# Performance work log

Measured on AMD Instinct MI355X. Metric: run time of the kernel, lower is better.

## Reference

```python
import jax, jax.numpy as jnp
import numpy as np

B, N, C = 8, 4096, 512
H = W = 64           # N = H * W, dimensionality == 2
SHIFT = 4            # shift_size
WS = 8               # window_size
R = 4                # mlp_ratio
EPS = 1e-6


def setup_inputs() -> dict:
    key = jax.random.key(0)
    ks = jax.random.split(key, 3)
    return {
        "inputs": jax.random.normal(ks[0], (B, N, C), dtype=jnp.float32),
        # second_norm (LayerNormalization) params
        "ln_gamma": jnp.ones((C,), jnp.float32),
        "ln_beta": jnp.zeros((C,), jnp.float32),
        # MLP params: Dense(C*R) -> gelu -> Dense(C)
        "W1": jax.random.normal(ks[1], (C, C * R), dtype=jnp.float32) * 0.02,
        "b1": jnp.zeros((C * R,), jnp.float32),
        "W2": jax.random.normal(ks[2], (C * R, C), dtype=jnp.float32) * 0.02,
        "b2": jnp.zeros((C,), jnp.float32),
    }


def _layer_norm(x, gamma, beta):
    mu = jnp.mean(x, axis=-1, keepdims=True)
    var = jnp.mean(jnp.square(x - mu), axis=-1, keepdims=True)
    return (x - mu) * jax.lax.rsqrt(var + EPS) * gamma + beta


def reference(inputs, ln_gamma, ln_beta, W1, b1, W2, b2):
    # NOTE: faithful to the provided call(): first_norm and attention are
    # never invoked (`normed = x`, `self_att = windowed`), so the window
    # partition + reverse is an exact identity round-trip of the shifted grid.
    grid = inputs.reshape(B, H, W, C)
    shifted = jnp.roll(grid, (-SHIFT, -SHIFT), axis=(1, 2))  # SwinCyclicShifter

    # window partition: [B, nH, nW, WS, WS, C] windows of WSxWS patches
    nh = H // WS
    win = shifted.reshape(B, nh, WS, nh, WS, C).transpose(0, 1, 3, 2, 4, 5)
    # (identity "attention" on [B*nH*nW, WS*WS, C]) then window reverse
    unwin = win.transpose(0, 1, 3, 2, 4, 5).reshape(B, N, C)

    x = unwin + inputs                       # residual add
    normed = _layer_norm(x, ln_gamma, ln_beta)
    h = jax.nn.gelu(normed @ W1 + b1)        # [B, N, 4C]
    mlp_out = h @ W2 + b2                    # [B, N, C]
    return mlp_out + x
```

## Files before the change

### kernel.cpp

```cpp
#include <hip/hip_runtime.h>
#include <hip/hip_bf16.h>
#include <cstdint>
#include <cstddef>


typedef short bf16x8 __attribute__((ext_vector_type(8)));
typedef float f32x4 __attribute__((ext_vector_type(4)));

#define GLOBAL_AS(p) ((__attribute__((address_space(1))) void*)(uintptr_t)(p))
#define LDS_AS(p)    ((__attribute__((address_space(3))) void*)(p))

static __device__ __forceinline__ ushort f2bf(float f) {
    uint32_t u = __float_as_uint(f);
    uint32_t r = (u + 0x7FFFu + ((u >> 16) & 1u)) >> 16;
    return (ushort)r;
}

static __device__ __forceinline__ float gelu_e2(float v) {
    float v2 = v * v;
    float m = fmaf(-0.1029433f, v2, -2.3022084f);
    float t = v * m;
    float e;
    asm("v_exp_f32 %0, %1" : "=v"(e) : "v"(t));
    return v * __builtin_amdgcn_rcpf(1.0f + e);
}

static __device__ __forceinline__ int rolled_row(int row) {
    int b = row >> 12, n = row & 4095;
    int h = n >> 6, wv = n & 63;
    int n2 = (((h + 4) & 63) << 6) | ((wv + 4) & 63);
    return (b << 12) | n2;
}

#define SBAR() do { __builtin_amdgcn_sched_barrier(0); \
                    __builtin_amdgcn_s_barrier(); \
                    __builtin_amdgcn_sched_barrier(0); } while (0)

#define LBAR() do { __builtin_amdgcn_sched_barrier(0); \
                    asm volatile("s_waitcnt lgkmcnt(0)" ::: "memory"); \
                    __builtin_amdgcn_s_barrier(); \
                    __builtin_amdgcn_sched_barrier(0); } while (0)

__global__ __launch_bounds__(128)
void ln_kernel(const float* __restrict__ in, const float* __restrict__ gamma,
               const float* __restrict__ beta, ushort* __restrict__ normed) {
    const int row = blockIdx.x;
    const int t = threadIdx.x;
    const int row2 = rolled_row(row);

    const float4* p0 = (const float4*)(in + (size_t)row * 512);
    const float4* p1 = (const float4*)(in + (size_t)row2 * 512);
    float4 a = p0[t], c = p1[t];
    float x0 = a.x + c.x, x1 = a.y + c.y, x2 = a.z + c.z, x3 = a.w + c.w;

    float s = x0 + x1 + x2 + x3;
    float sq = x0 * x0 + x1 * x1 + x2 * x2 + x3 * x3;
#pragma unroll
    for (int o = 32; o > 0; o >>= 1) {
        s += __shfl_xor(s, o);
        sq += __shfl_xor(sq, o);
    }
    __shared__ float red[4];
    if ((t & 63) == 0) { red[(t >> 6) * 2] = s; red[(t >> 6) * 2 + 1] = sq; }
    __syncthreads();
    s = red[0] + red[2];
    sq = red[1] + red[3];
    float mu = s * (1.0f / 512.0f);
    float var = sq * (1.0f / 512.0f) - mu * mu;
    float rs = rsqrtf(var + 1e-6f);

    float4 g = ((const float4*)gamma)[t];
    float4 be = ((const float4*)beta)[t];
    ushort4 o4;
    o4.x = f2bf((x0 - mu) * rs * g.x + be.x);
    o4.y = f2bf((x1 - mu) * rs * g.y + be.y);
    o4.z = f2bf((x2 - mu) * rs * g.z + be.z);
    o4.w = f2bf((x3 - mu) * rs * g.w + be.w);
    ((ushort4*)(normed + (size_t)row * 512))[t] = o4;
}

template <int PERM>
__global__ __launch_bounds__(256)
void transpose_cast(const float* __restrict__ src, ushort* __restrict__ dst,
                    int R, int Ccols) {
    __shared__ float tile[32][33];
    const int bx = blockIdx.x * 32;
    const int by = blockIdx.y * 32;
    const int tx = threadIdx.x, ty = threadIdx.y;
#pragma unroll
    for (int i = 0; i < 32; i += 8)
        tile[ty + i][tx] = src[(size_t)(by + ty + i) * Ccols + bx + tx];
    __syncthreads();
    int k = by + tx;
    int kd = PERM ? ((k & ~63) | ((k & 15) << 2) | ((k >> 4) & 3)) : k;
#pragma unroll
    for (int i = 0; i < 32; i += 8)
        dst[(size_t)(bx + ty + i) * R + kd] = f2bf(tile[tx][ty + i]);
}

__global__ __launch_bounds__(256)
void mlp_gemm1(const ushort* __restrict__ A, const ushort* __restrict__ Bt,
               const float* __restrict__ bias, ushort* __restrict__ outH) {
    constexpr int K = 512, N = 2048, BK = 64;
    __shared__ ushort Asm[128 * BK];
    __shared__ ushort Bsm[128 * BK];

    const int t = threadIdx.x;
    const int w = t >> 6, l = t & 63;
    const int wr = w >> 1, wc = w & 1;

    const int bid = blockIdx.x;
    const int xcd = bid & 7, idx = bid >> 3;
    const int brow = ((xcd << 5) + (idx >> 4)) << 7;
    const int bcol = (idx & 15) << 7;

    f32x4 acc[4][4] = {};

    const int trow = t >> 3;
    const int csrc = (((t & 7) ^ ((t >> 3) & 7)) << 3);
    const size_t aBase = (size_t)(brow + trow) * K + csrc;
    const size_t bBase = (size_t)(bcol + trow) * K + csrc;
    char* const ldsA = (char*)Asm + w * 1024;
    char* const ldsB = (char*)Bsm + w * 1024;

    const int rA = l & 15;
    const int cb0 = ((l >> 4) ^ (rA & 7)) << 4;
    const int bA0 = (wr << 13) + (rA << 7) + cb0;
    const int bB0 = (wc << 13) + (rA << 7) + cb0;
    const char* const pA0 = (const char*)Asm + bA0;
    const char* const pA1 = (const char*)Asm + (bA0 ^ 64);
    const char* const pB0 = (const char*)Bsm + bB0;
    const char* const pB1 = (const char*)Bsm + (bB0 ^ 64);

    for (int k0 = 0; k0 < K; k0 += BK) {
#pragma unroll
        for (int i = 0; i < 4; ++i) {
            __builtin_amdgcn_global_load_lds(GLOBAL_AS(A + aBase + (size_t)(i * 32) * K + k0),
                                             LDS_AS(ldsA + i * 4096), 16, 0, 0);
            __builtin_amdgcn_global_load_lds(GLOBAL_AS(Bt + bBase + (size_t)(i * 32) * K + k0),
                                             LDS_AS(ldsB + i * 4096), 16, 0, 0);
        }
        __syncthreads();

#pragma unroll
        for (int s = 0; s < 2; ++s) {
            const char* pa = s ? pA1 : pA0;
            const char* pb = s ? pB1 : pB0;
            bf16x8 aF[4], bF[4];
#pragma unroll
            for (int i = 0; i < 4; ++i)
                aF[i] = *(const bf16x8*)(pa + i * 2048);
#pragma unroll
            for (int j = 0; j < 4; ++j)
                bF[j] = *(const bf16x8*)(pb + j * 2048);
#pragma unroll
            for (int i = 0; i < 4; ++i)
#pragma unroll
                for (int j = 0; j < 4; ++j)
                    acc[i][j] = __builtin_amdgcn_mfma_f32_16x16x32_bf16(aF[i], bF[j], acc[i][j], 0, 0, 0);
        }
        __syncthreads();
    }

    const int cm = (l >> 4) << 2;
    const int cn = l & 15;
    float bvv[4];
#pragma unroll
    for (int j = 0; j < 4; ++j)
        bvv[j] = bias[bcol + wc * 64 + j * 16 + cn];
    const int ecol = bcol + wc * 64 + (cn << 2);
#pragma unroll
    for (int i = 0; i < 4; ++i) {
#pragma unroll
        for (int r = 0; r < 4; ++r) {
            const int row = brow + wr * 64 + i * 16 + cm + r;
            float f0 = gelu_e2(acc[i][0][r] + bvv[0]);
            float f1 = gelu_e2(acc[i][1][r] + bvv[1]);
            float f2 = gelu_e2(acc[i][2][r] + bvv[2]);
            float f3 = gelu_e2(acc[i][3][r] + bvv[3]);
            uint32_t lo, hi;
            asm("v_cvt_pk_bf16_f32 %0, %1, %2" : "=v"(lo) : "v"(f0), "v"(f1));
            asm("v_cvt_pk_bf16_f32 %0, %1, %2" : "=v"(hi) : "v"(f2), "v"(f3));
            uint2 pv; pv.x = lo; pv.y = hi;
            *(uint2*)(outH + (size_t)row * N + ecol) = pv;
        }
    }
}

__global__ __launch_bounds__(512, 2)
void mlp_gemm2(const ushort* __restrict__ A, const ushort* __restrict__ Bt,
               const float* __restrict__ bias, const float* __restrict__ resid,
               float* __restrict__ outF) {
    constexpr int KT = 2048, TT = 32, N = 512;
    __shared__ __align__(16) char sm[131072];
    const int t = threadIdx.x;
    const int w = t >> 6, l = t & 63;
    const int wr = w >> 2, wc = w & 3;

    const int nwg = gridDim.x;
    const int bid = blockIdx.x;
    const int swz = (bid & 7) * (nwg >> 3) + (bid >> 3);
    const int cb = swz & 1;
    const int rgrp = swz >> 1;
    const int brow0 = rgrp * 256;
    const int bcol = cb << 8;

    const int kksw = (((t & 3) ^ ((t >> 4) & 3)) << 3);
    const size_t aTh = (size_t)(t >> 2) * KT + kksw;
    const size_t bTh = (size_t)(bcol + (t >> 2)) * KT + kksw;
    const ushort* const aPanel = A + (size_t)brow0 * KT;
    char* const dA = (char*)sm + (w << 10);
    char* const dB = dA + 65536;

    const int xorv = ((l >> 2) & 3) << 4;
    const int preA = ((((wr << 7) + (l & 15)) << 6) + ((l >> 4) << 4)) ^ xorv;
    const int preB = 65536 + (((((wc << 6) + (l & 15)) << 6) + ((l >> 4) << 4)) ^ xorv);

    f32x4 acc[8][4] = {};
    bf16x8 aF[4], bF[4];

    auto issueA = [&](int T, int kh) {
        const int slot = ((T & 1) << 1) | kh;
        const ushort* s = aPanel + aTh + T * 64 + kh * 32;
        char* d = dA + (slot << 14);
        __builtin_amdgcn_global_load_lds(GLOBAL_AS(s), LDS_AS(d), 16, 0, 0);
        __builtin_amdgcn_global_load_lds(GLOBAL_AS(s + (size_t)128 * KT), LDS_AS(d + 8192), 16, 0, 0);
    };
    auto issueB = [&](int T, int kh) {
        const int slot = ((T & 1) << 1) | kh;
        const ushort* s = Bt + bTh + T * 64 + kh * 32;
        char* d = dB + (slot << 14);
        __builtin_amdgcn_global_load_lds(GLOBAL_AS(s), LDS_AS(d), 16, 0, 0);
        __builtin_amdgcn_global_load_lds(GLOBAL_AS(s + (size_t)128 * KT), LDS_AS(d + 8192), 16, 0, 0);
    };
    auto rdA = [&](int slot, int mb) {
        const char* p = (const char*)sm + (slot << 14) + preA + (mb << 12);
        aF[0] = *(const bf16x8*)(p);
        aF[1] = *(const bf16x8*)(p + 1024);
        aF[2] = *(const bf16x8*)(p + 2048);
        aF[3] = *(const bf16x8*)(p + 3072);
    };
    auto rdB = [&](int slot) {
        const char* p = (const char*)sm + (slot << 14) + preB;
        bF[0] = *(const bf16x8*)(p);
        bF[1] = *(const bf16x8*)(p + 1024);
        bF[2] = *(const bf16x8*)(p + 2048);
        bF[3] = *(const bf16x8*)(p + 3072);
    };
    auto mfma16 = [&](int mb) {
        __builtin_amdgcn_s_setprio(1);
#pragma unroll
        for (int mf = 0; mf < 4; ++mf)
#pragma unroll
            for (int nf = 0; nf < 4; ++nf)
                acc[mb * 4 + mf][nf] = __builtin_amdgcn_mfma_f32_16x16x32_bf16(
                    aF[mf], bF[nf], acc[mb * 4 + mf][nf], 0, 0, 0);
        __builtin_amdgcn_s_setprio(0);
    };

    auto tile_body = [&](int T) {
        const int s0 = (T & 1) << 1;
        rdA(s0, 0); rdB(s0);
        SBAR();
        if (T + 1 < TT) issueB(T + 1, 1);
        mfma16(0);
        SBAR();
        rdA(s0, 1);
        SBAR();
        if (T + 2 < TT) issueA(T + 2, 0);
        mfma16(1);
        SBAR();
        rdA(s0 + 1, 0); rdB(s0 + 1);
        SBAR();
        if (T + 2 < TT) issueB(T + 2, 0);
        mfma16(0);
        SBAR();
        rdA(s0 + 1, 1);
        SBAR();
        if (T + 2 < TT) issueA(T + 2, 1);
        mfma16(1);
        __builtin_amdgcn_sched_barrier(0);
        if (T < TT - 2)       { asm volatile("s_waitcnt vmcnt(6)" ::: "memory"); }
        else if (T == TT - 2) { asm volatile("s_waitcnt vmcnt(0)" ::: "memory"); }
        SBAR();
    };

    issueA(0, 0); issueB(0, 0);
    issueA(0, 1); issueB(0, 1);
    issueA(1, 0); issueB(1, 0);
    issueA(1, 1);
    __builtin_amdgcn_sched_barrier(0);
    asm volatile("s_waitcnt vmcnt(6)" ::: "memory");
    SBAR();

#pragma unroll 1
    for (int T = 0; T < TT; ++T)
        tile_body(T);

#pragma unroll
    for (int h2 = 0; h2 < 2; ++h2) {
        if (wr == h2) {
#pragma unroll
            for (int mf = 0; mf < 8; ++mf)
#pragma unroll
                for (int nf = 0; nf < 4; ++nf)
#pragma unroll
                    for (int r = 0; r < 4; ++r) {
                        int rl = mf * 16 + ((l >> 4) << 2) + r;
                        int col = (wc << 6) + nf * 16 + (l & 15);
                        *(float*)(sm + rl * 1024 + col * 4) = acc[mf][nf][r];
                    }
        }
        LBAR();
#pragma unroll
        for (int k = 0; k < 16; ++k) {
            int c = t + (k << 9);
            int row = c >> 6, c4 = c & 63;
            f32x4 v = *(const f32x4*)(sm + ((size_t)c << 4));
            int R = brow0 + (h2 << 7) + row;
            int col0 = bcol + (c4 << 2);
            f32x4 bb = *(const f32x4*)(bias + col0);
            f32x4 x0 = *(const f32x4*)(resid + (size_t)R * 512 + col0);
            f32x4 x1 = *(const f32x4*)(resid + (size_t)rolled_row(R) * 512 + col0);
            v = v + bb + x0 + x1;
            *(f32x4*)(outF + (size_t)R * N + col0) = v;
        }
        if (h2 == 0) LBAR();
    }
}

extern "C" void kernel_launch(void* const* d_in, const int* in_sizes, int n_in,
                              void* d_out, int out_size, void* d_ws, size_t ws_size,
                              hipStream_t stream) {
    const float* in = (const float*)d_in[0];
    const float* ln_g = (const float*)d_in[1];
    const float* ln_b = (const float*)d_in[2];
    const float* W1 = (const float*)d_in[3];
    const float* b1 = (const float*)d_in[4];
    const float* W2 = (const float*)d_in[5];
    const float* b2 = (const float*)d_in[6];
    float* out = (float*)d_out;

    char* ws = (char*)d_ws;
    ushort* normed = (ushort*)ws;
    ushort* hbuf   = (ushort*)(ws + (size_t)32 * 1024 * 1024);
    ushort* W1T    = (ushort*)(ws + (size_t)160 * 1024 * 1024);
    ushort* W2T    = (ushort*)(ws + (size_t)162 * 1024 * 1024);

    const int M = 32768;
    const int C = 512, C4 = 2048;

    ln_kernel<<<M, 128, 0, stream>>>(in, ln_g, ln_b, normed);
    transpose_cast<0><<<dim3(C4 / 32, C / 32), dim3(32, 8), 0, stream>>>(W1, W1T, C, C4);
    transpose_cast<1><<<dim3(C / 32, C4 / 32), dim3(32, 8), 0, stream>>>(W2, W2T, C4, C);

    mlp_gemm1<<<dim3(4096), 256, 0, stream>>>(normed, W1T, b1, hbuf);
    mlp_gemm2<<<dim3(256), 512, 0, stream>>>(hbuf, W2T, b2, in, out);
}
```

Before: 213.8 us.

## Load B operand fragments directly from global into registers in both GEMMs

Both MLP GEMM kernels stop staging the weight (B) tiles through LDS and instead load each wave's B fragments from global memory straight into registers. Each wave only needs its own columns, so this cuts LDS traffic and LDS footprint and changes the vmcnt bookkeeping in the pipelined second GEMM. In exchange, B rows that several waves share are now fetched repeatedly through L2/cache instead of once per block. The global loads are strided by row and may stall the MFMA stream if their latency is not hidden, especially in gemm1, where there is no prefetch.

```diff
diff --git a/kernel.cpp b/kernel.cpp
--- a/kernel.cpp
+++ b/kernel.cpp
@@ -103,7 +103,6 @@
                const float* __restrict__ bias, ushort* __restrict__ outH) {
     constexpr int K = 512, N = 2048, BK = 64;
     __shared__ ushort Asm[128 * BK];
-    __shared__ ushort Bsm[128 * BK];
 
     const int t = threadIdx.x;
     const int w = t >> 6, l = t & 63;
@@ -119,46 +118,47 @@
     const int trow = t >> 3;
     const int csrc = (((t & 7) ^ ((t >> 3) & 7)) << 3);
     const size_t aBase = (size_t)(brow + trow) * K + csrc;
-    const size_t bBase = (size_t)(bcol + trow) * K + csrc;
     char* const ldsA = (char*)Asm + w * 1024;
-    char* const ldsB = (char*)Bsm + w * 1024;
 
     const int rA = l & 15;
     const int cb0 = ((l >> 4) ^ (rA & 7)) << 4;
     const int bA0 = (wr << 13) + (rA << 7) + cb0;
-    const int bB0 = (wc << 13) + (rA << 7) + cb0;
     const char* const pA0 = (const char*)Asm + bA0;
     const char* const pA1 = (const char*)Asm + (bA0 ^ 64);
-    const char* const pB0 = (const char*)Bsm + bB0;
-    const char* const pB1 = (const char*)Bsm + (bB0 ^ 64);
+
+    const ushort* const bRow = Bt + (size_t)(bcol + wc * 64 + rA) * K + ((l >> 4) << 3);
 
     for (int k0 = 0; k0 < K; k0 += BK) {
-#pragma unroll
-        for (int i = 0; i < 4; ++i) {
+        bf16x8 bF0[4], bF1[4];
+#pragma unroll
+        for (int j = 0; j < 4; ++j) {
+            const ushort* p = bRow + (size_t)j * (16 * K) + k0;
+            bF0[j] = *(const bf16x8*)(p);
+            bF1[j] = *(const bf16x8*)(p + 32);
+        }
+#pragma unroll
+        for (int i = 0; i < 4; ++i)
             __builtin_amdgcn_global_load_lds(GLOBAL_AS(A + aBase + (size_t)(i * 32) * K + k0),
                                              LDS_AS(ldsA + i * 4096), 16, 0, 0);
-            __builtin_amdgcn_global_load_lds(GLOBAL_AS(Bt + bBase + (size_t)(i * 32) * K + k0),
-                                             LDS_AS(ldsB + i * 4096), 16, 0, 0);
-        }
         __syncthreads();
 
-#pragma unroll
-        for (int s = 0; s < 2; ++s) {
-            const char* pa = s ? pA1 : pA0;
-            const char* pb = s ? pB1 : pB0;
-            bf16x8 aF[4], bF[4];
-#pragma unroll
-            for (int i = 0; i < 4; ++i)
-                aF[i] = *(const bf16x8*)(pa + i * 2048);
+        bf16x8 aF[4];
+#pragma unroll
+        for (int i = 0; i < 4; ++i)
+            aF[i] = *(const bf16x8*)(pA0 + i * 2048);
+#pragma unroll
+        for (int i = 0; i < 4; ++i)
 #pragma unroll
             for (int j = 0; j < 4; ++j)
-                bF[j] = *(const bf16x8*)(pb + j * 2048);
-#pragma unroll
-            for (int i = 0; i < 4; ++i)
-#pragma unroll
-                for (int j = 0; j < 4; ++j)
-                    acc[i][j] = __builtin_amdgcn_mfma_f32_16x16x32_bf16(aF[i], bF[j], acc[i][j], 0, 0, 0);
-        }
+                acc[i][j] = __builtin_amdgcn_mfma_f32_16x16x32_bf16(aF[i], bF0[j], acc[i][j], 0, 0, 0);
+#pragma unroll
+        for (int i = 0; i < 4; ++i)
+            aF[i] = *(const bf16x8*)(pA1 + i * 2048);
+#pragma unroll
+        for (int i = 0; i < 4; ++i)
+#pragma unroll
+            for (int j = 0; j < 4; ++j)
+                acc[i][j] = __builtin_amdgcn_mfma_f32_16x16x32_bf16(aF[i], bF1[j], acc[i][j], 0, 0, 0);
         __syncthreads();
     }
 
@@ -207,17 +207,17 @@
 
     const int kksw = (((t & 3) ^ ((t >> 4) & 3)) << 3);
     const size_t aTh = (size_t)(t >> 2) * KT + kksw;
-    const size_t bTh = (size_t)(bcol + (t >> 2)) * KT + kksw;
     const ushort* const aPanel = A + (size_t)brow0 * KT;
     char* const dA = (char*)sm + (w << 10);
-    char* const dB = dA + 65536;
 
     const int xorv = ((l >> 2) & 3) << 4;
     const int preA = ((((wr << 7) + (l & 15)) << 6) + ((l >> 4) << 4)) ^ xorv;
-    const int preB = 65536 + (((((wc << 6) + (l & 15)) << 6) + ((l >> 4) << 4)) ^ xorv);
+
+    const ushort* const bRowG = Bt + (size_t)(bcol + (wc << 6) + (l & 15)) * KT + ((l >> 4) << 3);
 
     f32x4 acc[8][4] = {};
-    bf16x8 aF[4], bF[4];
+    bf16x8 aF[4];
+    bf16x8 bS0[4], bS1[4];
 
     auto issueA = [&](int T, int kh) {
         const int slot = ((T & 1) << 1) | kh;
@@ -226,12 +226,11 @@
         __builtin_amdgcn_global_load_lds(GLOBAL_AS(s), LDS_AS(d), 16, 0, 0);
         __builtin_amdgcn_global_load_lds(GLOBAL_AS(s + (size_t)128 * KT), LDS_AS(d + 8192), 16, 0, 0);
     };
-    auto issueB = [&](int T, int kh) {
-        const int slot = ((T & 1) << 1) | kh;
-        const ushort* s = Bt + bTh + T * 64 + kh * 32;
-        char* d = dB + (slot << 14);
-        __builtin_amdgcn_global_load_lds(GLOBAL_AS(s), LDS_AS(d), 16, 0, 0);
-        __builtin_amdgcn_global_load_lds(GLOBAL_AS(s + (size_t)128 * KT), LDS_AS(d + 8192), 16, 0, 0);
+    auto loadB = [&](int T, int kh, bf16x8* dst) {
+        const ushort* p = bRowG + T * 64 + kh * 32;
+#pragma unroll
+        for (int nf = 0; nf < 4; ++nf)
+            dst[nf] = *(const bf16x8*)(p + (size_t)nf * (16 * KT));
     };
     auto rdA = [&](int slot, int mb) {
         const char* p = (const char*)sm + (slot << 14) + preA + (mb << 12);
@@ -240,57 +239,49 @@
         aF[2] = *(const bf16x8*)(p + 2048);
         aF[3] = *(const bf16x8*)(p + 3072);
     };
-    auto rdB = [&](int slot) {
-        const char* p = (const char*)sm + (slot << 14) + preB;
-        bF[0] = *(const bf16x8*)(p);
-        bF[1] = *(const bf16x8*)(p + 1024);
-        bF[2] = *(const bf16x8*)(p + 2048);
-        bF[3] = *(const bf16x8*)(p + 3072);
-    };
-    auto mfma16 = [&](int mb) {
+    auto mfma16 = [&](int mb, const bf16x8* bf) {
         __builtin_amdgcn_s_setprio(1);
 #pragma unroll
         for (int mf = 0; mf < 4; ++mf)
 #pragma unroll
             for (int nf = 0; nf < 4; ++nf)
                 acc[mb * 4 + mf][nf] = __builtin_amdgcn_mfma_f32_16x16x32_bf16(
-                    aF[mf], bF[nf], acc[mb * 4 + mf][nf], 0, 0, 0);
+                    aF[mf], bf[nf], acc[mb * 4 + mf][nf], 0, 0, 0);
         __builtin_amdgcn_s_setprio(0);
     };
 
     auto tile_body = [&](int T) {
         const int s0 = (T & 1) << 1;
-        rdA(s0, 0); rdB(s0);
-        SBAR();
-        if (T + 1 < TT) issueB(T + 1, 1);
-        mfma16(0);
+        rdA(s0, 0);
+        SBAR();
+        loadB(T, 1, bS1);
+        mfma16(0, bS0);
         SBAR();
         rdA(s0, 1);
         SBAR();
         if (T + 2 < TT) issueA(T + 2, 0);
-        mfma16(1);
-        SBAR();
-        rdA(s0 + 1, 0); rdB(s0 + 1);
-        SBAR();
-        if (T + 2 < TT) issueB(T + 2, 0);
-        mfma16(0);
+        mfma16(1, bS0);
+        SBAR();
+        rdA(s0 + 1, 0);
+        SBAR();
+        mfma16(0, bS1);
         SBAR();
         rdA(s0 + 1, 1);
         SBAR();
         if (T + 2 < TT) issueA(T + 2, 1);
-        mfma16(1);
+        if (T + 1 < TT) loadB(T + 1, 0, bS0);
+        mfma16(1, bS1);
         __builtin_amdgcn_sched_barrier(0);
-        if (T < TT - 2)       { asm volatile("s_waitcnt vmcnt(6)" ::: "memory"); }
-        else if (T == TT - 2) { asm volatile("s_waitcnt vmcnt(0)" ::: "memory"); }
-        SBAR();
-    };
-
-    issueA(0, 0); issueB(0, 0);
-    issueA(0, 1); issueB(0, 1);
-    issueA(1, 0); issueB(1, 0);
-    issueA(1, 1);
+        if (T < TT - 2)       { asm volatile("s_waitcnt vmcnt(8)" ::: "memory"); }
+        else if (T == TT - 2) { asm volatile("s_waitcnt vmcnt(4)" ::: "memory"); }
+        SBAR();
+    };
+
+    issueA(0, 0); issueA(0, 1);
+    issueA(1, 0); issueA(1, 1);
+    loadB(0, 0, bS0);
     __builtin_amdgcn_sched_barrier(0);
-    asm volatile("s_waitcnt vmcnt(6)" ::: "memory");
+    asm volatile("s_waitcnt vmcnt(8)" ::: "memory");
     SBAR();
 
 #pragma unroll 1
```

Measured after the change: 304.9 us. +42.6%, slower.
